# Optimization experiments

Hardware: AMD Instinct MI355X
Metric: run time of the kernel (lower is better)

## Reference

```python
import jax, jax.numpy as jnp
import numpy as np

# Hyperparameters from init_kwargs (activation='sigmoid' => delta=7.0 per the module)
K = 64
EPS = 1e-4
N_ITERS = 10
BRANCH = 60
DELTA = 7.0


def setup_inputs() -> dict:
    key = jax.random.key(0)
    x = jax.random.normal(key, (16384, 256), dtype=jnp.float32)
    return {"x": x}


def _binnorm_forward(x):
    # x: [B, D]. Projects each row so that sum(sigmoid(x + nu)) == K via bisection on nu.
    B = x.shape[0]
    ls = jnp.linspace(0.0, 1.0, BRANCH, dtype=x.dtype)          # [branch]
    x_sorted = -jnp.sort(-x, axis=-1)                            # descending sort, [B, D]
    nu_lower = -x_sorted[:, K - 1] - DELTA                       # [B]
    nu_upper = -x_sorted[:, K] + DELTA                           # [B]
    b_idx = jnp.arange(B)
    r = nu_upper - nu_lower
    for _ in range(N_ITERS):
        r = nu_upper - nu_lower                                  # bracket width, [B]
        I = r > EPS                                              # rows still unconverged

        def rest(args):
            nl, nu_up = args
            nus = r[:, None] * ls + nl[:, None]                  # candidate nus, [B, branch]
            # fs[b, j] = sum_d sigmoid(x[b,d] + nus[b,j]) - K
            fs = jnp.sum(jax.nn.sigmoid(x[:, None, :] + nus[:, :, None]), axis=-1) - K  # [B, branch]
            cnt = jnp.sum((fs < 0).astype(jnp.int32), axis=-1)   # number of negative branches
            i_lo = cnt - 1
            J = i_lo < 0
            i_lo = jnp.where(J, 0, i_lo)
            i_hi = i_lo + 1
            nl2 = jnp.where(I, nus[b_idx, i_lo], nl)
            nu2 = jnp.where(I, nus[b_idx, i_hi], nu_up)
            nl2 = jnp.where(J, nl2 - DELTA, nl2)
            return (nl2, nu2)

        nu_lower, nu_upper = jax.lax.cond(jnp.any(I), rest, lambda a: a, (nu_lower, nu_upper))
    # NOTE: faithful to the original, nu uses r from the LAST iteration (pre-update)
    nu = nu_lower + r * 0.5
    return jax.nn.sigmoid(x + nu[:, None])


def reference(x):
    return _binnorm_forward(x)
```

## Files before the change

### kernel.cpp

```cpp
#include <hip/hip_runtime.h>


#define D_COLS 256
#define KF 64.0f
#define DELTA_F 7.0f
#define N_ITERS 8
#define LOG2E 1.44269504f

__global__ __launch_bounds__(256) void binnorm_kernel(const float* __restrict__ x,
                                                      float* __restrict__ out) {
    const int lane = threadIdx.x & 63;
    const int waveInBlock = threadIdx.x >> 6;
    const int j = lane & 15;
    const int rowLocal = lane >> 4;
    const int row = (blockIdx.x << 4) + (waveInBlock << 2) + rowLocal;

    const float4* xr = reinterpret_cast<const float4*>(x + (size_t)row * D_COLS);
    float4 c[4];
#pragma unroll
    for (int i = 0; i < 4; ++i) c[i] = xr[(i << 4) + j];

    float ev[16];
    float sum = 0.0f, mx = -1e30f, mn = 1e30f;
#pragma unroll
    for (int i = 0; i < 4; ++i) {
        const float q[4] = {c[i].x, c[i].y, c[i].z, c[i].w};
#pragma unroll
        for (int e = 0; e < 4; ++e) {
            const float xv = q[e];
            sum += xv;
            mx = fmaxf(mx, xv);
            mn = fminf(mn, xv);
            ev[(i << 2) + e] = __builtin_amdgcn_exp2f(-LOG2E * xv);
        }
    }
#pragma unroll
    for (int m = 1; m <= 8; m <<= 1) {
        sum += __shfl_xor(sum, m);
        mx = fmaxf(mx, __shfl_xor(mx, m));
        mn = fminf(mn, __shfl_xor(mn, m));
    }

    const float lo = -mx - DELTA_F;
    const float hi = -mn + DELTA_F;
    float nu = -1.09861229f - sum * (1.0f / 256.0f);
    nu = fminf(fmaxf(nu, lo + 1e-3f), hi - 1e-3f);

    float tlo = __builtin_amdgcn_exp2f(-LOG2E * hi);
    float thi = __builtin_amdgcn_exp2f(-LOG2E * lo);
    float t   = __builtin_amdgcn_exp2f(-LOG2E * nu);

    for (int it = 0; it < N_ITERS; ++it) {
        float f = 0.0f, fp = 0.0f;
#pragma unroll
        for (int e = 0; e < 16; ++e) {
            const float s = __builtin_amdgcn_rcpf(fmaf(ev[e], t, 1.0f));
            f += s;
            fp += fmaf(-s, s, s);
        }
#pragma unroll
        for (int m = 1; m <= 8; m <<= 1) {
            f += __shfl_xor(f, m);
            fp += __shfl_xor(fp, m);
        }
        f -= KF;
        if (f > 0.0f) tlo = t; else thi = t;
        float cand = fmaf(f * t, __builtin_amdgcn_rcpf(fp), t);
        if (!(cand >= tlo && cand <= thi)) cand = 0.5f * (tlo + thi);
        t = cand;
    }

    float4* orow = reinterpret_cast<float4*>(out + (size_t)row * D_COLS);
#pragma unroll
    for (int i = 0; i < 4; ++i) {
        float4 o;
        o.x = __builtin_amdgcn_rcpf(fmaf(ev[(i << 2) + 0], t, 1.0f));
        o.y = __builtin_amdgcn_rcpf(fmaf(ev[(i << 2) + 1], t, 1.0f));
        o.z = __builtin_amdgcn_rcpf(fmaf(ev[(i << 2) + 2], t, 1.0f));
        o.w = __builtin_amdgcn_rcpf(fmaf(ev[(i << 2) + 3], t, 1.0f));
        orow[(i << 4) + j] = o;
    }
}

extern "C" void kernel_launch(void* const* d_in, const int* in_sizes, int n_in,
                              void* d_out, int out_size, void* d_ws, size_t ws_size,
                              hipStream_t stream) {
    const float* x = (const float*)d_in[0];
    float* out = (float*)d_out;
    const int rows = 16384;
    binnorm_kernel<<<dim3(rows / 16), dim3(256), 0, stream>>>(x, out);
}
```

Baseline: 73.56 us.

## Use DPP row reductions, split accumulators, and early-exit Newton loop

Result: faster. 69.21 us (-5.9%).

```diff
diff --git a/kernel.cpp b/kernel.cpp
--- a/kernel.cpp
+++ b/kernel.cpp
@@ -6,6 +6,34 @@
 #define DELTA_F 7.0f
 #define N_ITERS 8
 #define LOG2E 1.44269504f
+
+template <int CTRL>
+__device__ __forceinline__ float dpp_mov(float v) {
+    return __int_as_float(__builtin_amdgcn_update_dpp(
+        0, __float_as_int(v), CTRL, 0xF, 0xF, true));
+}
+
+__device__ __forceinline__ float dpp_sum16(float v) {
+    v += dpp_mov<0xB1>(v);
+    v += dpp_mov<0x4E>(v);
+    v += dpp_mov<0x141>(v);
+    v += dpp_mov<0x140>(v);
+    return v;
+}
+__device__ __forceinline__ float dpp_max16(float v) {
+    v = fmaxf(v, dpp_mov<0xB1>(v));
+    v = fmaxf(v, dpp_mov<0x4E>(v));
+    v = fmaxf(v, dpp_mov<0x141>(v));
+    v = fmaxf(v, dpp_mov<0x140>(v));
+    return v;
+}
+__device__ __forceinline__ float dpp_min16(float v) {
+    v = fminf(v, dpp_mov<0xB1>(v));
+    v = fminf(v, dpp_mov<0x4E>(v));
+    v = fminf(v, dpp_mov<0x141>(v));
+    v = fminf(v, dpp_mov<0x140>(v));
+    return v;
+}
 
 __global__ __launch_bounds__(256) void binnorm_kernel(const float* __restrict__ x,
                                                       float* __restrict__ out) {
@@ -34,12 +62,9 @@
             ev[(i << 2) + e] = __builtin_amdgcn_exp2f(-LOG2E * xv);
         }
     }
-#pragma unroll
-    for (int m = 1; m <= 8; m <<= 1) {
-        sum += __shfl_xor(sum, m);
-        mx = fmaxf(mx, __shfl_xor(mx, m));
-        mn = fminf(mn, __shfl_xor(mn, m));
-    }
+    sum = dpp_sum16(sum);
+    mx = dpp_max16(mx);
+    mn = dpp_min16(mn);
 
     const float lo = -mx - DELTA_F;
     const float hi = -mn + DELTA_F;
@@ -51,19 +76,25 @@
     float t   = __builtin_amdgcn_exp2f(-LOG2E * nu);
 
     for (int it = 0; it < N_ITERS; ++it) {
-        float f = 0.0f, fp = 0.0f;
+        float f0 = 0.f, f1 = 0.f, f2 = 0.f, f3 = 0.f;
+        float p0 = 0.f, p1 = 0.f, p2 = 0.f, p3 = 0.f;
 #pragma unroll
-        for (int e = 0; e < 16; ++e) {
-            const float s = __builtin_amdgcn_rcpf(fmaf(ev[e], t, 1.0f));
-            f += s;
-            fp += fmaf(-s, s, s);
+        for (int e = 0; e < 4; ++e) {
+            float sa = __builtin_amdgcn_rcpf(fmaf(ev[4 * e + 0], t, 1.0f));
+            float sb = __builtin_amdgcn_rcpf(fmaf(ev[4 * e + 1], t, 1.0f));
+            float sc = __builtin_amdgcn_rcpf(fmaf(ev[4 * e + 2], t, 1.0f));
+            float sd = __builtin_amdgcn_rcpf(fmaf(ev[4 * e + 3], t, 1.0f));
+            f0 += sa; f1 += sb; f2 += sc; f3 += sd;
+            p0 = fmaf(-sa, sa, p0 + sa);
+            p1 = fmaf(-sb, sb, p1 + sb);
+            p2 = fmaf(-sc, sc, p2 + sc);
+            p3 = fmaf(-sd, sd, p3 + sd);
         }
-#pragma unroll
-        for (int m = 1; m <= 8; m <<= 1) {
-            f += __shfl_xor(f, m);
-            fp += __shfl_xor(fp, m);
-        }
-        f -= KF;
+        float f = dpp_sum16((f0 + f1) + (f2 + f3)) - KF;
+        float fp = dpp_sum16((p0 + p1) + (p2 + p3));
+
+        if (__all(fabsf(f) < 1e-3f)) break;
+
         if (f > 0.0f) tlo = t; else thi = t;
         float cand = fmaf(f * t, __builtin_amdgcn_rcpf(fp), t);
         if (!(cand >= tlo && cand <= thi)) cand = 0.5f * (tlo + thi);
```
